# Optimization experiments

Hardware: AMD Instinct MI355X
Metric: run time of the kernel (lower is better)

## Reference

```python
import jax, jax.numpy as jnp
import numpy as np

B, R, L, F, H = 65536, 12, 16, 8, 64  # batch, rss_dim, n_leds, led_feat_dim, head_dim

def setup_inputs() -> dict:
    key = jax.random.key(0)
    ks = jax.random.split(key, 20)
    p = lambda k, shp, s=0.1: (jax.random.normal(k, shp, dtype=jnp.float32) * s)
    return {
        "rss_t": jax.random.uniform(ks[0], (B, R, 1), dtype=jnp.float32),
        "led_features": jax.random.normal(ks[1], (B, L, F), dtype=jnp.float32),
        "led_positions": jax.random.normal(ks[2], (B, L, 3), dtype=jnp.float32),
        "prev_pos": jax.random.normal(ks[3], (B, 3), dtype=jnp.float32),
        "freq_mask": jax.random.randint(ks[4], (R, L), 0, 2).astype(jnp.int32),
        # intensity_gate: Linear(1,16) -> ReLU -> Linear(16,1) -> Sigmoid
        "gw1": p(ks[5], (1, 16)), "gb1": p(ks[6], (16,)),
        "gw2": p(ks[7], (16, 1)), "gb2": p(ks[8], (1,)),
        # query_proj: Linear(1,32) -> ReLU -> Linear(32,64)
        "qw1": p(ks[9], (1, 32)), "qb1": p(ks[10], (32,)),
        "qw2": p(ks[11], (32, H)), "qb2": p(ks[12], (H,)),
        # key_proj: Linear(F+3,32) -> ReLU -> Linear(32,64)
        "kw1": p(ks[13], (F + 3, 32)), "kb1": p(ks[14], (32,)),
        "kw2": p(ks[15], (32, H)), "kb2": p(ks[16], (H,)),
        "sigma": jnp.float32(0.5),
    }

def reference(rss_t, led_features, led_positions, prev_pos, freq_mask,
              gw1, gb1, gw2, gb2, qw1, qb1, qw2, qb2, kw1, kb1, kw2, kb2, sigma):
    # intensity gate with hard threshold
    gate = jax.nn.sigmoid(jax.nn.relu(rss_t @ gw1 + gb1) @ gw2 + gb2)  # [B,R,1]
    iw = (rss_t > 0.5).astype(rss_t.dtype) * gate                      # [B,R,1]
    # query / key projections
    Q = jax.nn.relu((rss_t * iw) @ qw1 + qb1) @ qw2 + qb2              # [B,R,H]
    led_input = jnp.concatenate([led_features, led_positions], axis=-1)  # [B,L,F+3]
    K = jax.nn.relu(led_input @ kw1 + kb1) @ kw2 + kb2                 # [B,L,H]
    scores = jnp.einsum("brh,blh->brl", Q, K)                          # [B,R,L]
    # distance bias
    dist_sq = jnp.sum((prev_pos[:, None, :] - led_positions) ** 2, axis=-1)  # [B,L]
    scores = scores - dist_sq[:, None, :] / (2.0 * sigma ** 2)
    # mask + softmax
    neg = jnp.finfo(scores.dtype).min
    scores = jnp.where(freq_mask[None, :, :] == 0, neg, scores)
    attn = jax.nn.softmax(scores, axis=-1)                             # [B,R,L]
    return attn, iw.squeeze(-1)
```

## Files before the change

kernel.cpp:

```cpp
#include <hip/hip_runtime.h>

#define B_TOT 65536
#define R 12
#define L 16
#define NB 16
#define NEG_MIN -3.402823466e38f

#define WS_V   0
#define WS_C   32
#define WS_PM  40
#define WS_BP  64
#define WS_TAB 96
#define TROW   72

typedef __attribute__((ext_vector_type(8))) short short8;
typedef __attribute__((ext_vector_type(4))) float f32x4;

static __device__ __forceinline__ short f2bf(float f) {
    uint32_t u = __float_as_uint(f);
    uint32_t r = u + 0x7FFFu + ((u >> 16) & 1u);
    return (short)(r >> 16);
}

static __device__ __forceinline__ unsigned cvt_pk_bf16(float a, float b) {
    unsigned d;
    asm("v_cvt_pk_bf16_f32 %0, %1, %2" : "=v"(d) : "v"(a), "v"(b));
    return d;
}

__global__ __launch_bounds__(256) void nfh_pre(
    const float* __restrict__ qw1, const float* __restrict__ qb1,
    const float* __restrict__ qw2, const float* __restrict__ qb2,
    const float* __restrict__ kw2, const float* __restrict__ kb2,
    const int*   __restrict__ fmask,
    float* __restrict__ ws)
{
    __shared__ float sM[1024];
    __shared__ float su[32];
    __shared__ float sw1[32], sb1[32], sbp[32];
    const int t = threadIdx.x;

    if (t < 32) { sw1[t] = qw1[t]; sb1[t] = qb1[t]; }
    for (int e = t; e < 1024; e += 256) {
        const int i = e >> 5, j = e & 31;
        float acc = 0.f;
        for (int h = 0; h < 64; ++h) acc = fmaf(qw2[i * 64 + h], kw2[j * 64 + h], acc);
        sM[e] = acc;
    }
    if (t < 32) {
        float au = 0.f, av = 0.f;
        for (int h = 0; h < 64; ++h) {
            au = fmaf(qw2[t * 64 + h], kb2[h], au);
            av = fmaf(kw2[t * 64 + h], qb2[h], av);
        }
        su[t] = au;
        ws[WS_V + t] = av;
        const float w = qw1[t];
        sbp[t] = (w != 0.f) ? (-qb1[t] / w) : 3.0e30f;
    }
    if (t == 64) {
        float acc = 0.f;
        for (int h = 0; h < 64; ++h) acc = fmaf(qb2[h], kb2[h], acc);
        ws[WS_C] = acc;
    }
    if (t < 12) {
        int pm = 0;
        for (int l = 0; l < 16; ++l) if (fmask[t * 16 + l] != 0) pm |= (1 << l);
        ((int*)ws)[WS_PM + t] = pm;
    }
    __syncthreads();
    if (t == 0) {
        for (int i = 1; i < 32; ++i) {
            float key = sbp[i]; int j = i - 1;
            while (j >= 0 && sbp[j] > key) { sbp[j + 1] = sbp[j]; --j; }
            sbp[j + 1] = key;
        }
    }
    __syncthreads();
    if (t < 32) ws[WS_BP + t] = sbp[t];

    for (int task = t; task < 33 * 32 + 33; task += 256) {
        const int m = (task < 33 * 32) ? (task >> 5) : (task - 33 * 32);
        const float xi = (m == 0) ? sbp[0] - 1.f
                       : ((m == 32) ? sbp[31] + 1.f
                                    : sbp[m - 1] + 0.5f * (sbp[m] - sbp[m - 1]));
        if (task < 33 * 32) {
            const int j = task & 31;
            float A = 0.f, Bv = 0.f;
            for (int i = 0; i < 32; ++i) {
                if (fmaf(sw1[i], xi, sb1[i]) > 0.f) {
                    A  = fmaf(sw1[i], sM[i * 32 + j], A);
                    Bv = fmaf(sb1[i], sM[i * 32 + j], Bv);
                }
            }
            ws[WS_TAB + m * TROW + j] = A;
            ws[WS_TAB + m * TROW + 36 + j] = Bv;
        } else {
            float Au = 0.f, Bu = 0.f;
            for (int i = 0; i < 32; ++i) {
                if (fmaf(sw1[i], xi, sb1[i]) > 0.f) {
                    Au = fmaf(sw1[i], su[i], Au);
                    Bu = fmaf(sb1[i], su[i], Bu);
                }
            }
            ws[WS_TAB + m * TROW + 32] = Au;
            ws[WS_TAB + m * TROW + 36 + 32] = Bu;
        }
    }
}

__global__ __launch_bounds__(256, 5) void nfh_main(
    const float* __restrict__ rss,
    const float* __restrict__ feat,
    const float* __restrict__ pos,
    const float* __restrict__ prev,
    const float* __restrict__ gw1, const float* __restrict__ gb1,
    const float* __restrict__ gw2, const float* __restrict__ gb2,
    const float* __restrict__ kw1, const float* __restrict__ kb1,
    const float* __restrict__ sigma_p,
    const float* __restrict__ ws,
    float* __restrict__ out)
{
    __shared__ short s_bhf[NB * 512];
    __shared__ short s_ttf[NB * 384];
    __shared__ float s_vb[NB * 16];
    __shared__ float s_tc[NB * 12];
    __shared__ int   s_pm[16];

    const int t = threadIdx.x;
    const int b0 = blockIdx.x * NB;
    const float sigma = sigma_p[0];
    const float inv2s2 = 1.f / (2.f * sigma * sigma);

    if (t < 16) s_pm[t] = (t < 12) ? ((const int*)ws)[WS_PM + t] : 0;

    {
        const int bb1 = t >> 4, l1 = t & 15;
        const int b = b0 + bb1;
        float in[11];
        const float4* f4 = (const float4*)(feat + ((size_t)b * (L * 8) + l1 * 8));
        const float4 fa = f4[0], fb = f4[1];
        in[0] = fa.x; in[1] = fa.y; in[2] = fa.z; in[3] = fa.w;
        in[4] = fb.x; in[5] = fb.y; in[6] = fb.z; in[7] = fb.w;
        const float* pp = pos + ((size_t)b * (L * 3) + l1 * 3);
        in[8] = pp[0]; in[9] = pp[1]; in[10] = pp[2];

        float dsq = 0.f;
        #pragma unroll
        for (int m = 0; m < 3; ++m) {
            const float d = prev[b * 3 + m] - in[8 + m];
            dsq = fmaf(d, d, dsq);
        }
        float bh[32];
        #pragma unroll
        for (int j = 0; j < 32; ++j) bh[j] = kb1[j];
        #pragma unroll
        for (int m = 0; m < 11; ++m) {
            const float im = in[m];
            #pragma unroll
            for (int j = 0; j < 32; ++j) bh[j] = fmaf(im, kw1[m * 32 + j], bh[j]);
        }
        float vb = ws[WS_C];
        #pragma unroll
        for (int j = 0; j < 32; ++j) {
            bh[j] = fmaxf(bh[j], 0.f);
            vb = fmaf(ws[WS_V + j], bh[j], vb);
        }
        s_vb[bb1 * 16 + l1] = vb - dsq * inv2s2;

        #pragma unroll
        for (int kb = 0; kb < 4; ++kb) {
            uint4 pk;
            pk.x = cvt_pk_bf16(bh[kb * 8 + 0], bh[kb * 8 + 1]);
            pk.y = cvt_pk_bf16(bh[kb * 8 + 2], bh[kb * 8 + 3]);
            pk.z = cvt_pk_bf16(bh[kb * 8 + 4], bh[kb * 8 + 5]);
            pk.w = cvt_pk_bf16(bh[kb * 8 + 6], bh[kb * 8 + 7]);
            *(uint4*)&s_bhf[bb1 * 512 + (kb * 16 + l1) * 8] = pk;
        }
    }

    if (t < NB * R) {
        const int bb2 = t / R;
        const int r2 = t - bb2 * R;
        const float x = rss[(size_t)b0 * R + t];
        float z = gb2[0];
        #pragma unroll
        for (int i = 0; i < 16; ++i) {
            const float h = fmaxf(fmaf(x, gw1[i], gb1[i]), 0.f);
            z = fmaf(h, gw2[i], z);
        }
        const float gate = 1.f / (1.f + __expf(-z));
        const float iw = (x > 0.5f) ? gate : 0.f;
        out[(size_t)B_TOT * R * L + (size_t)b0 * R + t] = iw;
        const float xq = x * iw;

        int k = 0;
        #pragma unroll
        for (int m = 0; m < 32; ++m) k += (xq > ws[WS_BP + m]) ? 1 : 0;
        const float* row = ws + WS_TAB + k * TROW;
        const float4* ra = (const float4*)row;
        const float4* rb = (const float4*)(row + 36);
        s_tc[bb2 * 12 + r2] = fmaf(xq, row[32], row[68]);
        #pragma unroll
        for (int kb = 0; kb < 4; ++kb) {
            const float4 a0 = ra[kb * 2], c0 = rb[kb * 2];
            const float4 a1 = ra[kb * 2 + 1], c1 = rb[kb * 2 + 1];
            uint4 pk;
            pk.x = cvt_pk_bf16(fmaf(xq, a0.x, c0.x), fmaf(xq, a0.y, c0.y));
            pk.y = cvt_pk_bf16(fmaf(xq, a0.z, c0.z), fmaf(xq, a0.w, c0.w));
            pk.z = cvt_pk_bf16(fmaf(xq, a1.x, c1.x), fmaf(xq, a1.y, c1.y));
            pk.w = cvt_pk_bf16(fmaf(xq, a1.z, c1.z), fmaf(xq, a1.w, c1.w));
            *(uint4*)&s_ttf[bb2 * 384 + (kb * 12 + r2) * 8] = pk;
        }
    }
    __syncthreads();

    {
        const int lane = t & 63;
        const int w = t >> 6;
        const int r = lane & 15;
        const int lg = lane >> 4;
        const int pm = s_pm[r];

        #pragma unroll
        for (int i = 0; i < 4; ++i) {
            const int bb = w * 4 + i;
            const short8 af = *(const short8*)&s_bhf[bb * 512 + lane * 8];
            short8 bf = (short8){0, 0, 0, 0, 0, 0, 0, 0};
            float tc = 0.f;
            if (r < R) {
                bf = *(const short8*)&s_ttf[bb * 384 + (lg * 12 + r) * 8];
                tc = s_tc[bb * 12 + r];
            }
            f32x4 acc = {0.f, 0.f, 0.f, 0.f};
            acc = __builtin_amdgcn_mfma_f32_16x16x32_bf16(af, bf, acc, 0, 0, 0);

            const f32x4 vb4 = *(const f32x4*)&s_vb[bb * 16 + lg * 4];

            float sc[4];
            #pragma unroll
            for (int j = 0; j < 4; ++j) {
                sc[j] = acc[j] + tc + vb4[j];
                if (!((pm >> (lg * 4 + j)) & 1)) sc[j] = NEG_MIN;
            }
            float mx = fmaxf(fmaxf(sc[0], sc[1]), fmaxf(sc[2], sc[3]));
            mx = fmaxf(mx, __shfl_xor(mx, 16));
            mx = fmaxf(mx, __shfl_xor(mx, 32));
            float sum = 0.f;
            #pragma unroll
            for (int j = 0; j < 4; ++j) { sc[j] = __expf(sc[j] - mx); sum += sc[j]; }
            sum += __shfl_xor(sum, 16);
            sum += __shfl_xor(sum, 32);
            const float inv = 1.f / sum;

            if (r < R) {
                float4* op = (float4*)(out + ((size_t)(b0 + bb) * R + r) * L + lg * 4);
                *op = make_float4(sc[0] * inv, sc[1] * inv, sc[2] * inv, sc[3] * inv);
            }
        }
    }
}

extern "C" void kernel_launch(void* const* d_in, const int* in_sizes, int n_in,
                              void* d_out, int out_size, void* d_ws, size_t ws_size,
                              hipStream_t stream) {
    const float* rss   = (const float*)d_in[0];
    const float* feat  = (const float*)d_in[1];
    const float* pos   = (const float*)d_in[2];
    const float* prev  = (const float*)d_in[3];
    const int*   fmask = (const int*)d_in[4];
    const float* gw1   = (const float*)d_in[5];
    const float* gb1   = (const float*)d_in[6];
    const float* gw2   = (const float*)d_in[7];
    const float* gb2   = (const float*)d_in[8];
    const float* qw1   = (const float*)d_in[9];
    const float* qb1   = (const float*)d_in[10];
    const float* qw2   = (const float*)d_in[11];
    const float* qb2   = (const float*)d_in[12];
    const float* kw1   = (const float*)d_in[13];
    const float* kb1   = (const float*)d_in[14];
    const float* kw2   = (const float*)d_in[15];
    const float* kb2   = (const float*)d_in[16];
    const float* sigma = (const float*)d_in[17];
    float* out = (float*)d_out;
    float* ws  = (float*)d_ws;

    nfh_pre<<<1, 256, 0, stream>>>(qw1, qb1, qw2, qb2, kw2, kb2, fmask, ws);
    nfh_main<<<B_TOT / NB, 256, 0, stream>>>(
        rss, feat, pos, prev,
        gw1, gb1, gw2, gb2, kw1, kb1,
        sigma, ws, out);
}
```

Baseline: 179.1 us.

## Compute key-projection first layer with split-bf16 MFMA instead of scalar FMAs

The per-LED first key layer (11x32 FMAs per thread) moves onto MFMA instructions. Inputs and weights are split into high and low bf16 parts so the products keep near-fp32 accuracy. The prepass kernel now packs the kw1/kb1 weight fragments into the workspace, and the main kernel computes ReLU, the v-dot reduction and the bf16 packing directly from MFMA outputs using lane shuffles. This is meant to remove the VALU-heavy scalar loop and its register pressure, at the cost of extra LDS staging, shuffles and four extra MFMAs per batch row. The occupancy hint also drops from 5 to 4.

Result: no change. 181.4 us (+1.3%).

```diff
diff --git a/kernel.cpp b/kernel.cpp
--- a/kernel.cpp
+++ b/kernel.cpp
@@ -12,6 +12,7 @@
 #define WS_BP  64
 #define WS_TAB 96
 #define TROW   72
+#define WS_WF  2472
 
 typedef __attribute__((ext_vector_type(8))) short short8;
 typedef __attribute__((ext_vector_type(4))) float f32x4;
@@ -32,6 +33,7 @@
     const float* __restrict__ qw1, const float* __restrict__ qb1,
     const float* __restrict__ qw2, const float* __restrict__ qb2,
     const float* __restrict__ kw2, const float* __restrict__ kb2,
+    const float* __restrict__ kw1, const float* __restrict__ kb1,
     const int*   __restrict__ fmask,
     float* __restrict__ ws)
 {
@@ -107,43 +109,80 @@
             ws[WS_TAB + m * TROW + 36 + 32] = Bu;
         }
     }
-}
-
-__global__ __launch_bounds__(256, 5) void nfh_main(
+
+    {
+        const int fr = t >> 6;
+        const int li = t & 63;
+        const int jl = li & 15, kb = li >> 4;
+        const int T = fr & 1, term = fr >> 1;
+        const int q = ((jl >> 2) << 3) + (T << 2) + (jl & 3);
+        short* wsp = (short*)(ws + WS_WF);
+        #pragma unroll
+        for (int e = 0; e < 8; ++e) {
+            const int k = kb * 8 + e;
+            float w = 0.f;
+            if (term == 0) {
+                if (k < 11)       w = kw1[k * 32 + q];
+                else if (k == 11) w = kb1[q];
+            } else {
+                if (k < 11)       w = kw1[k * 32 + q];
+                else if (k == 11) { const float b = kb1[q];
+                                    w = b - __uint_as_float(((uint32_t)(uint16_t)f2bf(b)) << 16); }
+                else if (k < 23)  { const float a = kw1[(k - 12) * 32 + q];
+                                    w = a - __uint_as_float(((uint32_t)(uint16_t)f2bf(a)) << 16); }
+            }
+            wsp[(fr * 64 + li) * 8 + e] = f2bf(w);
+        }
+    }
+}
+
+__global__ __launch_bounds__(256, 4) void nfh_main(
     const float* __restrict__ rss,
     const float* __restrict__ feat,
     const float* __restrict__ pos,
     const float* __restrict__ prev,
     const float* __restrict__ gw1, const float* __restrict__ gb1,
     const float* __restrict__ gw2, const float* __restrict__ gb2,
-    const float* __restrict__ kw1, const float* __restrict__ kb1,
     const float* __restrict__ sigma_p,
     const float* __restrict__ ws,
     float* __restrict__ out)
 {
-    __shared__ short s_bhf[NB * 512];
+    __shared__ short s_in[NB * 16 * 40 + 8];
     __shared__ short s_ttf[NB * 384];
-    __shared__ float s_vb[NB * 16];
+    __shared__ float s_dq[NB * 16];
     __shared__ float s_tc[NB * 12];
     __shared__ int   s_pm[16];
 
     const int t = threadIdx.x;
+    const int lane = t & 63;
+    const int lg = lane >> 4;
     const int b0 = blockIdx.x * NB;
     const float sigma = sigma_p[0];
     const float inv2s2 = 1.f / (2.f * sigma * sigma);
 
+    const short* wsp = (const short*)(ws + WS_WF);
+    const short8 wf0 = *(const short8*)(wsp + (0 * 64 + lane) * 8);
+    const short8 wf1 = *(const short8*)(wsp + (1 * 64 + lane) * 8);
+    const short8 wf2 = *(const short8*)(wsp + (2 * 64 + lane) * 8);
+    const short8 wf3 = *(const short8*)(wsp + (3 * 64 + lane) * 8);
+    const f32x4 v0 = *(const f32x4*)(ws + WS_V + lg * 8);
+    const f32x4 v1 = *(const f32x4*)(ws + WS_V + lg * 8 + 4);
+    const float cconst = ws[WS_C];
+
     if (t < 16) s_pm[t] = (t < 12) ? ((const int*)ws)[WS_PM + t] : 0;
+    if (t < 8)  s_in[NB * 16 * 40 + t] = 0;
 
     {
         const int bb1 = t >> 4, l1 = t & 15;
         const int b = b0 + bb1;
-        float in[11];
+        float in[12];
         const float4* f4 = (const float4*)(feat + ((size_t)b * (L * 8) + l1 * 8));
         const float4 fa = f4[0], fb = f4[1];
         in[0] = fa.x; in[1] = fa.y; in[2] = fa.z; in[3] = fa.w;
         in[4] = fb.x; in[5] = fb.y; in[6] = fb.z; in[7] = fb.w;
         const float* pp = pos + ((size_t)b * (L * 3) + l1 * 3);
         in[8] = pp[0]; in[9] = pp[1]; in[10] = pp[2];
+        in[11] = 1.0f;
 
         float dsq = 0.f;
         #pragma unroll
@@ -151,32 +190,26 @@
             const float d = prev[b * 3 + m] - in[8 + m];
             dsq = fmaf(d, d, dsq);
         }
-        float bh[32];
-        #pragma unroll
-        for (int j = 0; j < 32; ++j) bh[j] = kb1[j];
-        #pragma unroll
-        for (int m = 0; m < 11; ++m) {
-            const float im = in[m];
-            #pragma unroll
-            for (int j = 0; j < 32; ++j) bh[j] = fmaf(im, kw1[m * 32 + j], bh[j]);
-        }
-        float vb = ws[WS_C];
-        #pragma unroll
-        for (int j = 0; j < 32; ++j) {
-            bh[j] = fmaxf(bh[j], 0.f);
-            vb = fmaf(ws[WS_V + j], bh[j], vb);
-        }
-        s_vb[bb1 * 16 + l1] = vb - dsq * inv2s2;
-
-        #pragma unroll
-        for (int kb = 0; kb < 4; ++kb) {
-            uint4 pk;
-            pk.x = cvt_pk_bf16(bh[kb * 8 + 0], bh[kb * 8 + 1]);
-            pk.y = cvt_pk_bf16(bh[kb * 8 + 2], bh[kb * 8 + 3]);
-            pk.z = cvt_pk_bf16(bh[kb * 8 + 4], bh[kb * 8 + 5]);
-            pk.w = cvt_pk_bf16(bh[kb * 8 + 6], bh[kb * 8 + 7]);
-            *(uint4*)&s_bhf[bb1 * 512 + (kb * 16 + l1) * 8] = pk;
-        }
+        s_dq[bb1 * 16 + l1] = cconst - dsq * inv2s2;
+
+        unsigned hp[6], lp[6];
+        #pragma unroll
+        for (int p = 0; p < 6; ++p) {
+            const float a = in[2 * p], c = in[2 * p + 1];
+            const unsigned h = cvt_pk_bf16(a, c);
+            hp[p] = h;
+            const float h0 = __uint_as_float(h << 16);
+            const float h1 = __uint_as_float(h & 0xFFFF0000u);
+            lp[p] = cvt_pk_bf16(a - h0, c - h1);
+        }
+        const unsigned lp5m = (lp[5] & 0xFFFFu) | 0x3F800000u;
+
+        uint4* rowp = (uint4*)&s_in[(bb1 * 16 + l1) * 40];
+        rowp[0] = make_uint4(hp[0], hp[1], hp[2], hp[3]);
+        rowp[1] = make_uint4(hp[4], hp[5], 0u, 0u);
+        rowp[2] = make_uint4(lp[0], lp[1], lp[2], lp[3]);
+        rowp[3] = make_uint4(lp[4], lp5m, hp[0], hp[1]);
+        rowp[4] = make_uint4(hp[2], hp[3], hp[4], hp[5] & 0xFFFFu);
     }
 
     if (t < NB * R) {
@@ -216,16 +249,46 @@
     __syncthreads();
 
     {
-        const int lane = t & 63;
+        const int r = lane & 15;
         const int w = t >> 6;
-        const int r = lane & 15;
-        const int lg = lane >> 4;
         const int pm = s_pm[r];
 
         #pragma unroll
         for (int i = 0; i < 4; ++i) {
             const int bb = w * 4 + i;
-            const short8 af = *(const short8*)&s_bhf[bb * 512 + lane * 8];
+            const short* rowb = &s_in[(bb * 16 + r) * 40];
+            const short8 i1 = *(const short8*)(rowb + lg * 8);
+            const short8 i2 = *(const short8*)(rowb + 16 + lg * 8);
+
+            f32x4 d0 = {0.f, 0.f, 0.f, 0.f};
+            f32x4 d1 = {0.f, 0.f, 0.f, 0.f};
+            d0 = __builtin_amdgcn_mfma_f32_16x16x32_bf16(wf0, i1, d0, 0, 0, 0);
+            d0 = __builtin_amdgcn_mfma_f32_16x16x32_bf16(wf2, i2, d0, 0, 0, 0);
+            d1 = __builtin_amdgcn_mfma_f32_16x16x32_bf16(wf1, i1, d1, 0, 0, 0);
+            d1 = __builtin_amdgcn_mfma_f32_16x16x32_bf16(wf3, i2, d1, 0, 0, 0);
+
+            float vbp = 0.f;
+            #pragma unroll
+            for (int j = 0; j < 4; ++j) {
+                d0[j] = fmaxf(d0[j], 0.f);
+                vbp = fmaf(v0[j], d0[j], vbp);
+            }
+            #pragma unroll
+            for (int j = 0; j < 4; ++j) {
+                d1[j] = fmaxf(d1[j], 0.f);
+                vbp = fmaf(v1[j], d1[j], vbp);
+            }
+            vbp += __shfl_xor(vbp, 16);
+            vbp += __shfl_xor(vbp, 32);
+            const float vbl = vbp + s_dq[bb * 16 + r];
+
+            uint4 afp;
+            afp.x = cvt_pk_bf16(d0[0], d0[1]);
+            afp.y = cvt_pk_bf16(d0[2], d0[3]);
+            afp.z = cvt_pk_bf16(d1[0], d1[1]);
+            afp.w = cvt_pk_bf16(d1[2], d1[3]);
+            const short8 af = *(const short8*)&afp;
+
             short8 bf = (short8){0, 0, 0, 0, 0, 0, 0, 0};
             float tc = 0.f;
             if (r < R) {
@@ -235,12 +298,11 @@
             f32x4 acc = {0.f, 0.f, 0.f, 0.f};
             acc = __builtin_amdgcn_mfma_f32_16x16x32_bf16(af, bf, acc, 0, 0, 0);
 
-            const f32x4 vb4 = *(const f32x4*)&s_vb[bb * 16 + lg * 4];
-
             float sc[4];
             #pragma unroll
             for (int j = 0; j < 4; ++j) {
-                sc[j] = acc[j] + tc + vb4[j];
+                const float vbj = __shfl(vbl, lg * 4 + j);
+                sc[j] = acc[j] + tc + vbj;
                 if (!((pm >> (lg * 4 + j)) & 1)) sc[j] = NEG_MIN;
             }
             float mx = fmaxf(fmaxf(sc[0], sc[1]), fmaxf(sc[2], sc[3]));
@@ -285,9 +347,9 @@
     float* out = (float*)d_out;
     float* ws  = (float*)d_ws;
 
-    nfh_pre<<<1, 256, 0, stream>>>(qw1, qb1, qw2, qb2, kw2, kb2, fmask, ws);
+    nfh_pre<<<1, 256, 0, stream>>>(qw1, qb1, qw2, qb2, kw2, kb2, kw1, kb1, fmask, ws);
     nfh_main<<<B_TOT / NB, 256, 0, stream>>>(
         rss, feat, pos, prev,
-        gw1, gb1, gw2, gb2, kw1, kb1,
+        gw1, gb1, gw2, gb2,
         sigma, ws, out);
 }
```
